# Optimization experiments

Measured on AMD Instinct MI355X. Metric: run time of the kernel, lower is better.

The kernel has to match this reference:

```python
import jax, jax.numpy as jnp
import numpy as np

K = 30           # k for kNN graph in each DynamicEdgeConv
NS = 0.2         # LeakyReLU negative_slope used by the repo's MLP
N = 16384        # number of points
E = 262144       # number of candidate edges
IN_CH = 3


def _glorot(key, shape):
    fan_in, fan_out = shape
    s = jnp.sqrt(6.0 / (fan_in + fan_out))
    return jax.random.uniform(key, shape, minval=-s, maxval=s, dtype=jnp.float32)


def setup_inputs() -> dict:
    key = jax.random.key(0)
    ks = jax.random.split(key, 8)
    x = jax.random.normal(ks[0], (N, IN_CH), dtype=jnp.float32)
    edge_index = jax.random.randint(ks[1], (2, E), 0, N)
    return {
        "x": x,
        "edge_index": edge_index,
        # conv1: MLP([2*in_ch, 64])
        "W1": _glorot(ks[2], (2 * IN_CH, 64)), "b1": jnp.zeros((64,), jnp.float32),
        # conv2/conv3: MLP([2*64, 64])
        "W2": _glorot(ks[3], (128, 64)), "b2": jnp.zeros((64,), jnp.float32),
        "W3": _glorot(ks[4], (128, 64)), "b3": jnp.zeros((64,), jnp.float32),
        # edge head W = MLP([2*64, 64, 1])
        "Wh1": _glorot(ks[5], (128, 64)), "bh1": jnp.zeros((64,), jnp.float32),
        "Wh2": _glorot(ks[6], (64, 1)), "bh2": jnp.zeros((1,), jnp.float32),
    }


def _knn_idx(x, k):
    # kNN in feature space (includes self, as PyG's knn(x, x, k) does)
    sq = jnp.sum(x * x, axis=1)                       # [N]
    d = sq[:, None] + sq[None, :] - 2.0 * (x @ x.T)   # [N, N] squared distances
    return jax.lax.top_k(-d, k)[1]                    # [N, k]


def _edge_conv(x, W, b):
    # DynamicEdgeConv: per-neighbor MLP on [x_i, x_j - x_i], max aggregation
    idx = _knn_idx(x, K)                              # [N, K]
    xj = x[idx]                                       # [N, K, C]
    xi = jnp.broadcast_to(x[:, None, :], xj.shape)
    feat = jnp.concatenate([xi, xj - xi], axis=-1)    # [N, K, 2C]
    h = jax.nn.leaky_relu(feat @ W + b, NS)           # [N, K, 64]
    return jnp.max(h, axis=1)                         # [N, 64]


def reference(x, edge_index, W1, b1, W2, b2, W3, b3, Wh1, bh1, Wh2, bh2):
    x = _edge_conv(x, W1, b1)
    x = _edge_conv(x, W2, b2)
    x = _edge_conv(x, W3, b3)
    # torch.sort(edge_index, dim=0) canonicalizes each column (i<=j).
    # unique + inverse-gather is mathematically the identity on the per-edge
    # outputs (duplicate columns produce identical rows), so we compute the
    # edge head directly on the sorted (canonical) edges.
    v = jnp.sort(edge_index, axis=0)                  # [2, E]
    e = jnp.concatenate([x[v[0]], x[v[1]]], axis=1)   # [E, 128]
    h = jax.nn.leaky_relu(e @ Wh1 + bh1, NS)          # [E, 64]
    out = h @ Wh2 + bh2                               # [E, 1]
    return jax.nn.sigmoid(out).reshape(-1)            # [E]
```

## Files before the change

### kernel.cpp

```cpp
#include <hip/hip_runtime.h>
#include <cmath>

typedef __attribute__((ext_vector_type(8))) short bf16x8;
typedef __attribute__((ext_vector_type(4))) float f32x4;

constexpr int N_PTS = 16384;
constexpr int KK    = 30;
constexpr int NEDGE = 262144;
constexpr float NS  = 0.2f;
constexpr int S_SL  = 16;
constexpr int M_L   = 8;
constexpr int CPQ   = S_SL * 4 * M_L;

__device__ inline short f2bf_rne(float f) {
  unsigned u = __float_as_uint(f);
  unsigned r = (u + 0x7fffu + ((u >> 16) & 1u)) >> 16;
  return (short)r;
}

#define CEA(a, i, j) { unsigned lo_ = a[i] < a[j] ? a[i] : a[j]; \
                       unsigned hi_ = a[i] < a[j] ? a[j] : a[i]; \
                       a[i] = lo_; a[j] = hi_; }
#define SORT8(a) \
  CEA(a,0,1) CEA(a,2,3) CEA(a,4,5) CEA(a,6,7) \
  CEA(a,0,2) CEA(a,1,3) CEA(a,4,6) CEA(a,5,7) \
  CEA(a,1,2) CEA(a,5,6) \
  CEA(a,0,4) CEA(a,1,5) CEA(a,2,6) CEA(a,3,7) \
  CEA(a,2,4) CEA(a,3,5) \
  CEA(a,1,2) CEA(a,3,4) CEA(a,5,6)
#define MERGE8(kd, nk) \
  { _Pragma("unroll") for (int t_ = 0; t_ < 8; ++t_) { \
      unsigned v_ = nk[7 - t_]; kd[t_] = kd[t_] < v_ ? kd[t_] : v_; } } \
  CEA(kd,0,4) CEA(kd,1,5) CEA(kd,2,6) CEA(kd,3,7) \
  CEA(kd,0,2) CEA(kd,1,3) CEA(kd,4,6) CEA(kd,5,7) \
  CEA(kd,0,1) CEA(kd,2,3) CEA(kd,4,5) CEA(kd,6,7)

#define ROR_ADD(x, N) \
  { float t_ = __int_as_float(__builtin_amdgcn_update_dpp( \
        0, __float_as_int(x), 0x120 + (N), 0xF, 0xF, 0)); (x) += t_; }

template<int C, int CP>
__global__ __launch_bounds__(256) void sqhi(const float* __restrict__ X,
    float* __restrict__ sqv, short* __restrict__ Xh) {
  int p = blockIdx.x * 256 + threadIdx.x;
  float s = 0.f;
#pragma unroll
  for (int c = 0; c < C; ++c) {
    float v = X[(size_t)p * C + c];
    s = fmaf(v, v, s);
    Xh[(size_t)p * CP + c] = f2bf_rne(v);
  }
#pragma unroll
  for (int c = C; c < CP; ++c) Xh[(size_t)p * CP + c] = 0;
  sqv[p] = s;
}

template<int KT>
__global__ __launch_bounds__(256) void knn_pass1(
    const short* __restrict__ Xh, const float* __restrict__ sqv,
    unsigned short* __restrict__ cand) {
  constexpr int CP = KT * 32;
  const int tid  = threadIdx.x;
  const int lane = tid & 63;
  const int wv   = tid >> 6;
  const int col  = lane & 15;
  const int quad = lane >> 4;
  const int qb   = blockIdx.x * 256 + wv * 64 + col;
  const int slice = blockIdx.y;
  const int slen = N_PTS / S_SL;
  const int c0 = slice * slen;

  bf16x8 bq[4][KT];
#pragma unroll
  for (int g = 0; g < 4; ++g)
#pragma unroll
    for (int kt = 0; kt < KT; ++kt)
      bq[g][kt] = *(const bf16x8*)(Xh + (size_t)(qb + g * 16) * CP + kt * 32 + quad * 8);

  unsigned kd0[M_L], kd1[M_L], kd2[M_L], kd3[M_L];
#pragma unroll
  for (int t = 0; t < M_L; ++t) {
    kd0[t] = 0xFFFFFFFFu; kd1[t] = 0xFFFFFFFFu;
    kd2[t] = 0xFFFFFFFFu; kd3[t] = 0xFFFFFFFFu;
  }

  const int NB = slen / 32;
  for (int bt = 0; bt < NB; ++bt) {
    const int cb = c0 + bt * 32;
    const size_t arow0 = (size_t)(cb + col) * CP + quad * 8;
    const size_t arow1 = arow0 + (size_t)16 * CP;
    unsigned nk0[8], nk1[8], nk2[8], nk3[8];
    {
      bf16x8 ah[KT];
#pragma unroll
      for (int kt = 0; kt < KT; ++kt)
        ah[kt] = *(const bf16x8*)(Xh + arow0 + kt * 32);
      f32x4 a0 = {0.f,0.f,0.f,0.f}, a1 = {0.f,0.f,0.f,0.f};
      f32x4 a2 = {0.f,0.f,0.f,0.f}, a3 = {0.f,0.f,0.f,0.f};
#pragma unroll
      for (int kt = 0; kt < KT; ++kt) {
        a0 = __builtin_amdgcn_mfma_f32_16x16x32_bf16(ah[kt], bq[0][kt], a0, 0, 0, 0);
        a1 = __builtin_amdgcn_mfma_f32_16x16x32_bf16(ah[kt], bq[1][kt], a1, 0, 0, 0);
        a2 = __builtin_amdgcn_mfma_f32_16x16x32_bf16(ah[kt], bq[2][kt], a2, 0, 0, 0);
        a3 = __builtin_amdgcn_mfma_f32_16x16x32_bf16(ah[kt], bq[3][kt], a3, 0, 0, 0);
      }
      f32x4 sc = *(const f32x4*)(sqv + cb + quad * 4);
      const unsigned lb = (unsigned)bt * 8;
#pragma unroll
      for (int r = 0; r < 4; ++r) {
        unsigned u0 = __float_as_uint(fmaf(a0[r], -2.f, sc[r]));
        unsigned u1 = __float_as_uint(fmaf(a1[r], -2.f, sc[r]));
        unsigned u2 = __float_as_uint(fmaf(a2[r], -2.f, sc[r]));
        unsigned u3 = __float_as_uint(fmaf(a3[r], -2.f, sc[r]));
        u0 ^= ((unsigned)((int)u0 >> 31)) | 0x80000000u;
        u1 ^= ((unsigned)((int)u1 >> 31)) | 0x80000000u;
        u2 ^= ((unsigned)((int)u2 >> 31)) | 0x80000000u;
        u3 ^= ((unsigned)((int)u3 >> 31)) | 0x80000000u;
        nk0[r] = (u0 & 0xFFFFFF00u) | (lb + r);
        nk1[r] = (u1 & 0xFFFFFF00u) | (lb + r);
        nk2[r] = (u2 & 0xFFFFFF00u) | (lb + r);
        nk3[r] = (u3 & 0xFFFFFF00u) | (lb + r);
      }
    }
    {
      bf16x8 ah[KT];
#pragma unroll
      for (int kt = 0; kt < KT; ++kt)
        ah[kt] = *(const bf16x8*)(Xh + arow1 + kt * 32);
      f32x4 a0 = {0.f,0.f,0.f,0.f}, a1 = {0.f,0.f,0.f,0.f};
      f32x4 a2 = {0.f,0.f,0.f,0.f}, a3 = {0.f,0.f,0.f,0.f};
#pragma unroll
      for (int kt = 0; kt < KT; ++kt) {
        a0 = __builtin_amdgcn_mfma_f32_16x16x32_bf16(ah[kt], bq[0][kt], a0, 0, 0, 0);
        a1 = __builtin_amdgcn_mfma_f32_16x16x32_bf16(ah[kt], bq[1][kt], a1, 0, 0, 0);
        a2 = __builtin_amdgcn_mfma_f32_16x16x32_bf16(ah[kt], bq[2][kt], a2, 0, 0, 0);
        a3 = __builtin_amdgcn_mfma_f32_16x16x32_bf16(ah[kt], bq[3][kt], a3, 0, 0, 0);
      }
      f32x4 sc = *(const f32x4*)(sqv + cb + 16 + quad * 4);
      const unsigned lb = (unsigned)bt * 8 + 4;
#pragma unroll
      for (int r = 0; r < 4; ++r) {
        unsigned u0 = __float_as_uint(fmaf(a0[r], -2.f, sc[r]));
        unsigned u1 = __float_as_uint(fmaf(a1[r], -2.f, sc[r]));
        unsigned u2 = __float_as_uint(fmaf(a2[r], -2.f, sc[r]));
        unsigned u3 = __float_as_uint(fmaf(a3[r], -2.f, sc[r]));
        u0 ^= ((unsigned)((int)u0 >> 31)) | 0x80000000u;
        u1 ^= ((unsigned)((int)u1 >> 31)) | 0x80000000u;
        u2 ^= ((unsigned)((int)u2 >> 31)) | 0x80000000u;
        u3 ^= ((unsigned)((int)u3 >> 31)) | 0x80000000u;
        nk0[4 + r] = (u0 & 0xFFFFFF00u) | (lb + r);
        nk1[4 + r] = (u1 & 0xFFFFFF00u) | (lb + r);
        nk2[4 + r] = (u2 & 0xFFFFFF00u) | (lb + r);
        nk3[4 + r] = (u3 & 0xFFFFFF00u) | (lb + r);
      }
    }
    SORT8(nk0) MERGE8(kd0, nk0)
    SORT8(nk1) MERGE8(kd1, nk1)
    SORT8(nk2) MERGE8(kd2, nk2)
    SORT8(nk3) MERGE8(kd3, nk3)
  }

#pragma unroll
  for (int g = 0; g < 4; ++g) {
    const unsigned* kd = (g == 0) ? kd0 : (g == 1) ? kd1 : (g == 2) ? kd2 : kd3;
    unsigned short* o =
        cand + ((size_t)(qb + g * 16) * S_SL + slice) * (4 * M_L) + quad * M_L;
#pragma unroll
    for (int t = 0; t < M_L; ++t) {
      unsigned l = kd[t] & 0xFFu;
      o[t] = (unsigned short)(c0 + (int)(l >> 2) * 16 + quad * 4 + (int)(l & 3));
    }
  }
}

__global__ __launch_bounds__(256) void knn_pass2v2(
    const float* __restrict__ X, const float* __restrict__ sqv,
    const unsigned short* __restrict__ cand, int* __restrict__ knn) {
  __shared__ int   ldsC[4][CPQ];
  __shared__ float ldsD[4][CPQ];
  const int lane = threadIdx.x & 63, wv = threadIdx.x >> 6;
  const int q = blockIdx.x * 4 + wv;
  const int s = lane & 15;
  const int g = lane >> 4;
  const float sqq = sqv[q];
  constexpr int PL = CPQ / 64;

#pragma unroll
  for (int u = 0; u < PL; ++u)
    ldsC[wv][u * 64 + lane] = (int)cand[(size_t)q * CPQ + u * 64 + lane];
  f32x4 xq = *(const f32x4*)(X + (size_t)q * 64 + s * 4);
  __syncthreads();

  for (int it = 0; it < CPQ / 16; ++it) {
    int jj[4];
#pragma unroll
    for (int uu = 0; uu < 4; ++uu) jj[uu] = ldsC[wv][it * 16 + uu * 4 + g];
    f32x4 vv[4];
#pragma unroll
    for (int uu = 0; uu < 4; ++uu)
      vv[uu] = *(const f32x4*)(X + (size_t)jj[uu] * 64 + s * 4);
    float sj[4];
#pragma unroll
    for (int uu = 0; uu < 4; ++uu) sj[uu] = sqv[jj[uu]];
#pragma unroll
    for (int uu = 0; uu < 4; ++uu) {
      float p = fmaf(xq[0], vv[uu][0], fmaf(xq[1], vv[uu][1],
                fmaf(xq[2], vv[uu][2], xq[3] * vv[uu][3])));
      ROR_ADD(p, 8) ROR_ADD(p, 4) ROR_ADD(p, 2) ROR_ADD(p, 1)
      if (s == 0) ldsD[wv][it * 16 + uu * 4 + g] = (sqq + sj[uu]) - 2.f * p;
    }
  }
  __syncthreads();

  float d[PL]; int id[PL];
#pragma unroll
  for (int u = 0; u < PL; ++u) {
    d[u]  = ldsD[wv][u * 64 + lane];
    id[u] = ldsC[wv][u * 64 + lane];
  }
  for (int r = 0; r < KK; ++r) {
    float bd = d[0]; int bi = id[0];
#pragma unroll
    for (int u = 1; u < PL; ++u) {
      bool c = (d[u] < bd) || (d[u] == bd && id[u] < bi);
      bd = c ? d[u] : bd; bi = c ? id[u] : bi;
    }
#pragma unroll
    for (int off = 32; off; off >>= 1) {
      float od = __shfl_xor(bd, off, 64);
      int   oi = __shfl_xor(bi, off, 64);
      bool c = (od < bd) || (od == bd && oi < bi);
      bd = c ? od : bd; bi = c ? oi : bi;
    }
    if (lane == 0) knn[(size_t)q * KK + r] = bi;
#pragma unroll
    for (int u = 0; u < PL; ++u) if (id[u] == bi) d[u] = __builtin_inff();
  }
}

template<int C, int GRP, int LG>
__global__ __launch_bounds__(256) void knn_pass2co(
    const float* __restrict__ X, const float* __restrict__ sqv,
    const unsigned short* __restrict__ cand, int* __restrict__ knn) {
  __shared__ float ldsD[4][CPQ];
  const int lane = threadIdx.x & 63, wv = threadIdx.x >> 6;
  const int q = blockIdx.x * 4 + wv;
  const int s = lane & (GRP - 1);
  const int g = lane >> LG;
  constexpr int RPI = 64 / GRP;
  constexpr int NIT = CPQ / RPI;
  const float sqq = sqv[q];

  float xqv[4];
  if constexpr (GRP == 16) {
#pragma unroll
    for (int u = 0; u < 4; ++u) xqv[u] = X[(size_t)q * C + s * 4 + u];
  } else {
    xqv[0] = (s < C) ? X[(size_t)q * C + s] : 0.f;
  }

  for (int it = 0; it < NIT; ++it) {
    const int t = it * RPI + g;
    const int j = (int)cand[(size_t)q * CPQ + t];
    float p;
    if constexpr (GRP == 16) {
      f32x4 v = *(const f32x4*)(X + (size_t)j * C + s * 4);
      p = fmaf(xqv[0], v[0], fmaf(xqv[1], v[1], fmaf(xqv[2], v[2], xqv[3] * v[3])));
    } else {
      float v = (s < C) ? X[(size_t)j * C + s] : 0.f;
      p = xqv[0] * v;
    }
#pragma unroll
    for (int off = 1; off < GRP; off <<= 1) p += __shfl_xor(p, off, 64);
    if (s == 0) ldsD[wv][t] = (sqq + sqv[j]) - 2.f * p;
  }
  __syncthreads();

  constexpr int PL = CPQ / 64;
  float d[PL]; int id[PL];
#pragma unroll
  for (int u = 0; u < PL; ++u) {
    d[u]  = ldsD[wv][u * 64 + lane];
    id[u] = (int)cand[(size_t)q * CPQ + u * 64 + lane];
  }
  for (int r = 0; r < KK; ++r) {
    float bd = d[0]; int bi = id[0];
#pragma unroll
    for (int u = 1; u < PL; ++u) {
      bool c = (d[u] < bd) || (d[u] == bd && id[u] < bi);
      bd = c ? d[u] : bd; bi = c ? id[u] : bi;
    }
#pragma unroll
    for (int off = 32; off; off >>= 1) {
      float od = __shfl_xor(bd, off, 64);
      int   oi = __shfl_xor(bi, off, 64);
      bool c = (od < bd) || (od == bd && oi < bi);
      bd = c ? od : bd; bi = c ? oi : bi;
    }
    if (lane == 0) knn[(size_t)q * KK + r] = bi;
#pragma unroll
    for (int u = 0; u < PL; ++u) if (id[u] == bi) d[u] = __builtin_inff();
  }
}

template<int C, int PPW>
__global__ __launch_bounds__(256) void edge_conv(
    const float* __restrict__ X, const int* __restrict__ knn,
    const float* __restrict__ W, const float* __restrict__ B,
    float* __restrict__ Y) {
  const int wv = __builtin_amdgcn_readfirstlane(threadIdx.x >> 6);
  const int lane = threadIdx.x & 63;
  float wd[C], wj[C];
#pragma unroll
  for (int c = 0; c < C; ++c) {
    float w0 = W[c * 64 + lane];
    float w1 = W[(C + c) * 64 + lane];
    wd[c] = w0 - w1; wj[c] = w1;
  }
  const float bb = B[lane];
  const int p0 = (blockIdx.x * 4 + wv) * PPW;
  for (int pp = 0; pp < PPW; ++pp) {
    const int p = p0 + pp;
    const float* __restrict__ xi = X + (size_t)p * C;
    float base = bb;
#pragma unroll
    for (int c = 0; c < C; ++c) base = fmaf(xi[c], wd[c], base);
    float m = -__builtin_inff();
    for (int n = 0; n < KK; ++n) {
      const int j = __builtin_amdgcn_readfirstlane(knn[(size_t)p * KK + n]);
      const float* __restrict__ xj = X + (size_t)j * C;
      float acc;
      if constexpr (C % 4 == 0) {
        float a0 = 0.f, a1 = 0.f, a2 = 0.f, a3 = 0.f;
#pragma unroll
        for (int c = 0; c < C; c += 4) {
          a0 = fmaf(xj[c + 0], wj[c + 0], a0);
          a1 = fmaf(xj[c + 1], wj[c + 1], a1);
          a2 = fmaf(xj[c + 2], wj[c + 2], a2);
          a3 = fmaf(xj[c + 3], wj[c + 3], a3);
        }
        acc = base + ((a0 + a1) + (a2 + a3));
      } else {
        acc = base;
#pragma unroll
        for (int c = 0; c < C; ++c) acc = fmaf(xj[c], wj[c], acc);
      }
      acc = acc > 0.f ? acc : NS * acc;
      m = fmaxf(m, acc);
    }
    Y[(size_t)p * 64 + lane] = m;
  }
}

template<int EPW>
__global__ __launch_bounds__(256) void edge_head(
    const float* __restrict__ X, const int* __restrict__ ei,
    const float* __restrict__ Wh1, const float* __restrict__ bh1,
    const float* __restrict__ Wh2, const float* __restrict__ bh2,
    float* __restrict__ out) {
  const int wv = __builtin_amdgcn_readfirstlane(threadIdx.x >> 6);
  const int lane = threadIdx.x & 63;
  float w0[64], w1[64];
#pragma unroll
  for (int c = 0; c < 64; ++c) {
    w0[c] = Wh1[c * 64 + lane];
    w1[c] = Wh1[(64 + c) * 64 + lane];
  }
  const float bb = bh1[lane];
  const float wv2 = Wh2[lane];
  const float b2 = bh2[0];
  const int e0 = (blockIdx.x * 4 + wv) * EPW;
  for (int ee = 0; ee < EPW; ++ee) {
    const int e = e0 + ee;
    const int a = ei[e], b = ei[NEDGE + e];
    const int v0 = __builtin_amdgcn_readfirstlane(min(a, b));
    const int v1 = __builtin_amdgcn_readfirstlane(max(a, b));
    const float* __restrict__ f0 = X + (size_t)v0 * 64;
    const float* __restrict__ f1 = X + (size_t)v1 * 64;
    float a0 = 0.f, a1 = 0.f, a2 = 0.f, a3 = 0.f;
#pragma unroll
    for (int c = 0; c < 64; c += 4) {
      a0 = fmaf(f0[c + 0], w0[c + 0], a0);
      a1 = fmaf(f0[c + 1], w0[c + 1], a1);
      a2 = fmaf(f0[c + 2], w0[c + 2], a2);
      a3 = fmaf(f0[c + 3], w0[c + 3], a3);
    }
#pragma unroll
    for (int c = 0; c < 64; c += 4) {
      a0 = fmaf(f1[c + 0], w1[c + 0], a0);
      a1 = fmaf(f1[c + 1], w1[c + 1], a1);
      a2 = fmaf(f1[c + 2], w1[c + 2], a2);
      a3 = fmaf(f1[c + 3], w1[c + 3], a3);
    }
    float h = bb + ((a0 + a1) + (a2 + a3));
    h = h > 0.f ? h : NS * h;
    float z = h * wv2;
#pragma unroll
    for (int off = 32; off; off >>= 1) z += __shfl_xor(z, off, 64);
    if (lane == 0) out[e] = 1.f / (1.f + expf(-(z + b2)));
  }
}

extern "C" void kernel_launch(void* const* d_in, const int* in_sizes, int n_in,
                              void* d_out, int out_size, void* d_ws, size_t ws_size,
                              hipStream_t stream) {
  const float* x   = (const float*)d_in[0];
  const int*   ei  = (const int*)d_in[1];
  const float* W1  = (const float*)d_in[2];
  const float* b1  = (const float*)d_in[3];
  const float* W2  = (const float*)d_in[4];
  const float* b2  = (const float*)d_in[5];
  const float* W3  = (const float*)d_in[6];
  const float* b3  = (const float*)d_in[7];
  const float* Wh1 = (const float*)d_in[8];
  const float* bh1 = (const float*)d_in[9];
  const float* Wh2 = (const float*)d_in[10];
  const float* bh2 = (const float*)d_in[11];
  float* out = (float*)d_out;

  char* ws = (char*)d_ws;
  float* xA  = (float*)ws; ws += (size_t)N_PTS * 64 * 4;
  float* xB  = (float*)ws; ws += (size_t)N_PTS * 64 * 4;
  float* sqb = (float*)ws; ws += (size_t)N_PTS * 4;
  int*   knn = (int*)ws;   ws += (size_t)N_PTS * KK * 4;
  short* Xh  = (short*)ws; ws += (size_t)N_PTS * 64 * 2;
  unsigned short* cand = (unsigned short*)ws;
  ws += (size_t)N_PTS * CPQ * 2;
  (void)ws_size; (void)in_sizes; (void)n_in; (void)out_size;

  sqhi<3, 32><<<N_PTS / 256, 256, 0, stream>>>(x, sqb, Xh);
  knn_pass1<1><<<dim3(N_PTS / 256, S_SL), 256, 0, stream>>>(Xh, sqb, cand);
  knn_pass2co<3, 4, 2><<<N_PTS / 4, 256, 0, stream>>>(x, sqb, cand, knn);
  edge_conv<3, 4><<<N_PTS / 16, 256, 0, stream>>>(x, knn, W1, b1, xA);
  sqhi<64, 64><<<N_PTS / 256, 256, 0, stream>>>(xA, sqb, Xh);
  knn_pass1<2><<<dim3(N_PTS / 256, S_SL), 256, 0, stream>>>(Xh, sqb, cand);
  knn_pass2v2<<<N_PTS / 4, 256, 0, stream>>>(xA, sqb, cand, knn);
  edge_conv<64, 4><<<N_PTS / 16, 256, 0, stream>>>(xA, knn, W2, b2, xB);
  sqhi<64, 64><<<N_PTS / 256, 256, 0, stream>>>(xB, sqb, Xh);
  knn_pass1<2><<<dim3(N_PTS / 256, S_SL), 256, 0, stream>>>(Xh, sqb, cand);
  knn_pass2v2<<<N_PTS / 4, 256, 0, stream>>>(xB, sqb, cand, knn);
  edge_conv<64, 4><<<N_PTS / 16, 256, 0, stream>>>(xB, knn, W3, b3, xA);
  edge_head<16><<<NEDGE / 64, 256, 0, stream>>>(xA, ei, Wh1, bh1, Wh2, bh2, out);
}
```

Before: 1.226 ms.

## Replace bf16 MFMA kNN first pass for 3-D input with scalar fp32 scan

For the first layer (3 input channels), the bf16 MFMA candidate pass padded to 32 channels is replaced by a scalar per-thread fp32 scan. Each thread computes distances with FMAs and keeps per-quarter top-8 candidates via sorting networks. Separately, the pass-2 selection loop now pre-sorts each lane's 8 candidates once and pops from the head, instead of doing a linear min and invalidation every round. This trades the padded matrix-core work and repeated scans for more scalar ALU work and register pressure.

```diff
diff --git a/kernel.cpp b/kernel.cpp
--- a/kernel.cpp
+++ b/kernel.cpp
@@ -35,9 +35,30 @@
   CEA(kd,0,2) CEA(kd,1,3) CEA(kd,4,6) CEA(kd,5,7) \
   CEA(kd,0,1) CEA(kd,2,3) CEA(kd,4,5) CEA(kd,6,7)
 
+#define CEP(i, j) { bool c_ = (d[i] < d[j]) || (d[i] == d[j] && id[i] < id[j]); \
+  float dl_ = c_ ? d[i] : d[j], dh_ = c_ ? d[j] : d[i]; \
+  int   il_ = c_ ? id[i] : id[j], ih_ = c_ ? id[j] : id[i]; \
+  d[i] = dl_; d[j] = dh_; id[i] = il_; id[j] = ih_; }
+#define SORTP8() \
+  CEP(0,1) CEP(2,3) CEP(4,5) CEP(6,7) \
+  CEP(0,2) CEP(1,3) CEP(4,6) CEP(5,7) \
+  CEP(1,2) CEP(5,6) \
+  CEP(0,4) CEP(1,5) CEP(2,6) CEP(3,7) \
+  CEP(2,4) CEP(3,5) \
+  CEP(1,2) CEP(3,4) CEP(5,6)
+
 #define ROR_ADD(x, N) \
   { float t_ = __int_as_float(__builtin_amdgcn_update_dpp( \
         0, __float_as_int(x), 0x120 + (N), 0xF, 0xF, 0)); (x) += t_; }
+
+__global__ __launch_bounds__(256) void sq3(const float* __restrict__ X,
+                                           float* __restrict__ sqv) {
+  int p = blockIdx.x * 256 + threadIdx.x;
+  float s = 0.f;
+#pragma unroll
+  for (int c = 0; c < 3; ++c) { float v = X[(size_t)p * 3 + c]; s = fmaf(v, v, s); }
+  sqv[p] = s;
+}
 
 template<int C, int CP>
 __global__ __launch_bounds__(256) void sqhi(const float* __restrict__ X,
@@ -53,6 +74,50 @@
 #pragma unroll
   for (int c = C; c < CP; ++c) Xh[(size_t)p * CP + c] = 0;
   sqv[p] = s;
+}
+
+__global__ __launch_bounds__(256) void knn_scan3(
+    const float* __restrict__ X, const float* __restrict__ sqv,
+    unsigned short* __restrict__ cand) {
+  const int q = blockIdx.x * 256 + threadIdx.x;
+  const int slice = blockIdx.y;
+  const int c0 = slice * 1024;
+  const float x0 = X[(size_t)q * 3 + 0];
+  const float x1 = X[(size_t)q * 3 + 1];
+  const float x2 = X[(size_t)q * 3 + 2];
+
+  unsigned kq0[8], kq1[8], kq2[8], kq3[8];
+#pragma unroll
+  for (int t = 0; t < 8; ++t) { kq0[t]=0xFFFFFFFFu; kq1[t]=0xFFFFFFFFu;
+                                kq2[t]=0xFFFFFFFFu; kq3[t]=0xFFFFFFFFu; }
+
+#define SCAN_QTR(kd, QO) \
+  for (int t = 0; t < 256; t += 8) { \
+    unsigned nk[8]; \
+    _Pragma("unroll") for (int u = 0; u < 8; ++u) { \
+      const int j = c0 + (QO) * 256 + t + u; \
+      float dj = fmaf(x0, X[(size_t)j*3+0], fmaf(x1, X[(size_t)j*3+1], x2 * X[(size_t)j*3+2])); \
+      float key = fmaf(dj, -2.f, sqv[j]); \
+      unsigned uu = __float_as_uint(key); \
+      uu ^= ((unsigned)((int)uu >> 31)) | 0x80000000u; \
+      nk[u] = (uu & 0xFFFFFF00u) | (unsigned)(t + u); \
+    } \
+    SORT8(nk) MERGE8(kd, nk) \
+  }
+  SCAN_QTR(kq0, 0)
+  SCAN_QTR(kq1, 1)
+  SCAN_QTR(kq2, 2)
+  SCAN_QTR(kq3, 3)
+#undef SCAN_QTR
+
+  unsigned short* o = cand + (size_t)q * CPQ + slice * 32;
+#pragma unroll
+  for (int t = 0; t < 8; ++t) {
+    o[t]      = (unsigned short)(c0 +   0 + (int)(kq0[t] & 0xFFu));
+    o[8 + t]  = (unsigned short)(c0 + 256 + (int)(kq1[t] & 0xFFu));
+    o[16 + t] = (unsigned short)(c0 + 512 + (int)(kq2[t] & 0xFFu));
+    o[24 + t] = (unsigned short)(c0 + 768 + (int)(kq3[t] & 0xFFu));
+  }
 }
 
 template<int KT>
@@ -218,13 +283,9 @@
     d[u]  = ldsD[wv][u * 64 + lane];
     id[u] = ldsC[wv][u * 64 + lane];
   }
+  SORTP8();
   for (int r = 0; r < KK; ++r) {
     float bd = d[0]; int bi = id[0];
-#pragma unroll
-    for (int u = 1; u < PL; ++u) {
-      bool c = (d[u] < bd) || (d[u] == bd && id[u] < bi);
-      bd = c ? d[u] : bd; bi = c ? id[u] : bi;
-    }
 #pragma unroll
     for (int off = 32; off; off >>= 1) {
       float od = __shfl_xor(bd, off, 64);
@@ -233,8 +294,13 @@
       bd = c ? od : bd; bi = c ? oi : bi;
     }
     if (lane == 0) knn[(size_t)q * KK + r] = bi;
-#pragma unroll
-    for (int u = 0; u < PL; ++u) if (id[u] == bi) d[u] = __builtin_inff();
+    bool win = (d[0] == bd) && (id[0] == bi);
+#pragma unroll
+    for (int t = 0; t < PL - 1; ++t) {
+      d[t]  = win ? d[t + 1]  : d[t];
+      id[t] = win ? id[t + 1] : id[t];
+    }
+    d[PL - 1] = win ? __builtin_inff() : d[PL - 1];
   }
 }
 
@@ -428,8 +494,8 @@
   ws += (size_t)N_PTS * CPQ * 2;
   (void)ws_size; (void)in_sizes; (void)n_in; (void)out_size;
 
-  sqhi<3, 32><<<N_PTS / 256, 256, 0, stream>>>(x, sqb, Xh);
-  knn_pass1<1><<<dim3(N_PTS / 256, S_SL), 256, 0, stream>>>(Xh, sqb, cand);
+  sq3<<<N_PTS / 256, 256, 0, stream>>>(x, sqb);
+  knn_scan3<<<dim3(N_PTS / 256, S_SL), 256, 0, stream>>>(x, sqb, cand);
   knn_pass2co<3, 4, 2><<<N_PTS / 4, 256, 0, stream>>>(x, sqb, cand, knn);
   edge_conv<3, 4><<<N_PTS / 16, 256, 0, stream>>>(x, knn, W1, b1, xA);
   sqhi<64, 64><<<N_PTS / 256, 256, 0, stream>>>(xA, sqb, Xh);
```

Result: no change. 1.208 ms (-1.4%).
